# Performance work log

Hardware: AMD Instinct MI355X
Metric: run time of the kernel (lower is better)

## Reference

```python
import jax, jax.numpy as jnp
import numpy as np

N = 50000
E = 800000
D = 64  # d_s


def _mlp2(x, w1, b1, w2, b2):
    # Linear -> SiLU -> Linear
    return jax.nn.silu(x @ w1 + b1) @ w2 + b2


def setup_inputs() -> dict:
    key = jax.random.key(0)
    ks = jax.random.split(key, 20)
    s = jax.random.normal(ks[0], (N, D), jnp.float32)
    v = jax.random.normal(ks[1], (N, 3), jnp.float32)
    edge_index = jax.random.randint(ks[2], (2, E), 0, N, jnp.int32)
    edge_attr = jax.random.normal(ks[3], (E, D), jnp.float32)
    ev = jax.random.normal(ks[4], (E, 3), jnp.float32)
    edge_vec_unit = ev / jnp.linalg.norm(ev, axis=-1, keepdims=True)

    def lin(k, fan_in, fan_out):
        kw, kb = jax.random.split(k)
        lim = 1.0 / np.sqrt(fan_in)
        w = jax.random.uniform(kw, (fan_in, fan_out), jnp.float32, -lim, lim)
        b = jax.random.uniform(kb, (fan_out,), jnp.float32, -lim, lim)
        return w, b

    ng_w1, ng_b1 = lin(ks[5], D + 1, D)
    ng_w2, ng_b2 = lin(ks[6], D, D)
    eg_w1, eg_b1 = lin(ks[7], D + 1, D)
    eg_w2, eg_b2 = lin(ks[8], D, D)
    mg_w1, mg_b1 = lin(ks[9], 3 * D, 2 * D)
    mg_w2, mg_b2 = lin(ks[10], 2 * D, D)
    pe_w, pe_b = lin(ks[11], D, 1)
    up_w, up_b = lin(ks[12], D, D)
    ln_g = jnp.ones((D,), jnp.float32)
    ln_b = jnp.zeros((D,), jnp.float32)
    return dict(s=s, v=v, edge_index=edge_index, edge_attr=edge_attr,
                edge_vec_unit=edge_vec_unit,
                ng_w1=ng_w1, ng_b1=ng_b1, ng_w2=ng_w2, ng_b2=ng_b2,
                eg_w1=eg_w1, eg_b1=eg_b1, eg_w2=eg_w2, eg_b2=eg_b2,
                mg_w1=mg_w1, mg_b1=mg_b1, mg_w2=mg_w2, mg_b2=mg_b2,
                pe_w=pe_w, pe_b=pe_b, up_w=up_w, up_b=up_b,
                ln_g=ln_g, ln_b=ln_b)


def reference(s, v, edge_index, edge_attr, edge_vec_unit,
              ng_w1, ng_b1, ng_w2, ng_b2,
              eg_w1, eg_b1, eg_w2, eg_b2,
              mg_w1, mg_b1, mg_w2, mg_b2,
              pe_w, pe_b, up_w, up_b, ln_g, ln_b):
    row, col = edge_index[0], edge_index[1]
    s_i, s_j = s[row], s[col]            # (E, D)
    v_i, v_j = v[row], v[col]            # (E, 3)

    dot_ij = jnp.sum(v_i * edge_vec_unit, axis=-1, keepdims=True)
    dot_ji = jnp.sum(v_j * -edge_vec_unit, axis=-1, keepdims=True)
    res_ij = 1.0 - dot_ij
    res_ji = 1.0 - dot_ji
    cross_mag = jnp.linalg.norm(jnp.cross(v_i, v_j), axis=-1, keepdims=True)

    node_feat_i = _mlp2(jnp.concatenate([s_i, res_ij], -1), ng_w1, ng_b1, ng_w2, ng_b2)
    node_feat_j = _mlp2(jnp.concatenate([s_j, res_ji], -1), ng_w1, ng_b1, ng_w2, ng_b2)
    edge_feat = _mlp2(jnp.concatenate([edge_attr, cross_mag], -1), eg_w1, eg_b1, eg_w2, eg_b2)

    msg = _mlp2(jnp.concatenate([node_feat_i, node_feat_j, edge_feat], -1),
                mg_w1, mg_b1, mg_w2, mg_b2)   # (E, D)
    coeff = msg @ pe_w + pe_b                 # (E, 1)
    v_msg = edge_vec_unit * coeff             # (E, 3)

    n = s.shape[0]
    s_agg = jax.ops.segment_sum(msg, row, num_segments=n)    # (N, D)
    v_agg = jax.ops.segment_sum(v_msg, row, num_segments=n)  # (N, 3)

    s_new = s + jax.nn.silu(s_agg) @ up_w + up_b
    mu = jnp.mean(s_new, axis=-1, keepdims=True)
    var = jnp.var(s_new, axis=-1, keepdims=True)
    s_out = (s_new - mu) * jax.lax.rsqrt(var + 1e-5) * ln_g + ln_b

    v_new = v + v_agg
    denom = jnp.maximum(jnp.linalg.norm(v_new, axis=-1, keepdims=True), 1e-6)
    v_out = v_new / denom
    return (s_out, v_out)
```

## Files before the change

kernel.cpp:

```cpp
#include <hip/hip_runtime.h>
#include <math.h>

#define NN 50000
#define NE 800000
#define D 64
#define TILE 64

typedef __attribute__((ext_vector_type(8))) short short8;
typedef __attribute__((ext_vector_type(4))) float f32x4;

__device__ __forceinline__ float rdlane(float x, int k) {
  return __uint_as_float(__builtin_amdgcn_readlane(__float_as_uint(x), k));
}
__device__ __forceinline__ float silu_f(float x) { return x / (1.0f + __expf(-x)); }
__device__ __forceinline__ float bfly_sum(float x) {
#pragma unroll
  for (int off = 32; off >= 1; off >>= 1) x += __shfl_xor(x, off, 64);
  return x;
}
__device__ __forceinline__ unsigned short f2bf(float f) {
  unsigned int u = __float_as_uint(f);
  u += 0x7fffu + ((u >> 16) & 1u);
  return (unsigned short)(u >> 16);
}
__device__ __forceinline__ unsigned int pack2(float a, float b) {
  return (unsigned int)f2bf(a) | ((unsigned int)f2bf(b) << 16);
}

__global__ void prep_all(const float* __restrict__ ng_w2,
                         const float* __restrict__ eg_w1,
                         const float* __restrict__ eg_w2,
                         const float* __restrict__ mg_w1,
                         const float* __restrict__ mg_w2,
                         unsigned short* __restrict__ out) {
  int t = blockIdx.x * 256 + threadIdx.x;
  if (t >= 88 * 64) return;
  int frag = t >> 6, L = t & 63;
  const float* W; int K, N, f0;
  if (frag < 8)       { W = ng_w2; K = 64;  N = 64;  f0 = 0; }
  else if (frag < 16) { W = eg_w1; K = 64;  N = 64;  f0 = 8; }
  else if (frag < 24) { W = eg_w2; K = 64;  N = 64;  f0 = 16; }
  else if (frag < 72) { W = mg_w1; K = 192; N = 128; f0 = 24; }
  else                { W = mg_w2; K = 128; N = 64;  f0 = 72; }
  int lf = frag - f0;
  int kd = K >> 5;
  int nt = lf / kd, ks = lf % kd;
  int kb = ks * 32 + (L >> 4) * 8;
  int nc = nt * 16 + (L & 15);
  unsigned int p[4];
#pragma unroll
  for (int jj = 0; jj < 4; ++jj) {
    float a = W[(size_t)(kb + 2 * jj) * N + nc];
    float b = W[(size_t)(kb + 2 * jj + 1) * N + nc];
    p[jj] = pack2(a, b);
  }
  *(uint4*)(out + (size_t)frag * 512 + L * 8) = make_uint4(p[0], p[1], p[2], p[3]);
}

__global__ void node_pre_kernel(const float* __restrict__ s,
                                const float* __restrict__ ng_w1,
                                const float* __restrict__ ng_b1,
                                float* __restrict__ h_ng) {
  int wave = blockIdx.x * (blockDim.x >> 6) + (threadIdx.x >> 6);
  int d = threadIdx.x & 63;
  int n0 = wave * 2;
  if (n0 >= NN) return;
  float x0 = s[(size_t)n0 * D + d];
  float x1 = (n0 + 1 < NN) ? s[(size_t)(n0 + 1) * D + d] : 0.f;
  float b = ng_b1[d];
  float a0 = b, a1 = b;
#pragma unroll 16
  for (int k = 0; k < D; ++k) {
    float w = ng_w1[k * D + d];
    a0 += rdlane(x0, k) * w;
    a1 += rdlane(x1, k) * w;
  }
  h_ng[(size_t)n0 * D + d] = a0;
  if (n0 + 1 < NN) h_ng[(size_t)(n0 + 1) * D + d] = a1;
}

#define OFF_XE 0
#define OFF_AE 9216
#define OFF_A0 0
#define OFF_A1 9216
#define OFF_H  0
#define OFF_C1 18432
#define OFF_ROW 44032
#define OFF_COL 44288
#define OFF_RIJ 44544
#define OFF_RJI 44800
#define OFF_CMG 45056
#define OFF_U   45312
#define OFF_CP  46080
#define SM_SIZE 47104
#define SA 144
#define SC 400
#define SH 272

__global__ __launch_bounds__(256, 3) void edge_mfma(
    const float* __restrict__ v, const int* __restrict__ ei,
    const float* __restrict__ edge_attr, const float* __restrict__ evu,
    const float* __restrict__ ng_w1, const float* __restrict__ ng_b2,
    const float* __restrict__ eg_w1, const float* __restrict__ eg_b1,
    const float* __restrict__ eg_b2,
    const float* __restrict__ mg_b1, const float* __restrict__ mg_b2,
    const float* __restrict__ pe_w, const float* __restrict__ pe_b,
    const float* __restrict__ h_ng,
    const unsigned short* __restrict__ WF,
    float* __restrict__ s_agg, float* __restrict__ v_agg) {
  __shared__ __align__(16) char sm[SM_SIZE];
  int tid = threadIdx.x;
  int w = tid >> 6, lane = tid & 63, l15 = lane & 15, quad = lane >> 4;
  int edge0 = blockIdx.x * TILE;

  short8 F_ng[2], F_e1[2], F_e2[2], F_m1[2][6], F_m2[4];
#pragma unroll
  for (int k = 0; k < 2; ++k) {
    F_ng[k] = *(const short8*)(WF + (size_t)(0 + w * 2 + k) * 512 + lane * 8);
    F_e1[k] = *(const short8*)(WF + (size_t)(8 + w * 2 + k) * 512 + lane * 8);
    F_e2[k] = *(const short8*)(WF + (size_t)(16 + w * 2 + k) * 512 + lane * 8);
  }
#pragma unroll
  for (int n2 = 0; n2 < 2; ++n2)
#pragma unroll
    for (int k = 0; k < 6; ++k)
      F_m1[n2][k] = *(const short8*)(WF + (size_t)(24 + (2 * w + n2) * 6 + k) * 512 + lane * 8);
#pragma unroll
  for (int k = 0; k < 4; ++k)
    F_m2[k] = *(const short8*)(WF + (size_t)(72 + w * 4 + k) * 512 + lane * 8);

  int col = w * 16 + l15;
  float b_ng2 = ng_b2[col];
  float b_e1 = eg_b1[col], b_e2 = eg_b2[col];
  float eglast = eg_w1[64 * 64 + col];
  float b_m1a = mg_b1[w * 32 + l15], b_m1b = mg_b1[w * 32 + 16 + l15];
  float b_m2 = mg_b2[col];
  float pw = pe_w[col];
  float peb = pe_b[0];

  if (tid < 64) {
    int e = tid, ed = edge0 + e;
    int r = ei[ed], c = ei[NE + ed];
    float u0 = evu[ed * 3 + 0], u1 = evu[ed * 3 + 1], u2 = evu[ed * 3 + 2];
    float vi0 = v[r * 3 + 0], vi1 = v[r * 3 + 1], vi2 = v[r * 3 + 2];
    float vj0 = v[c * 3 + 0], vj1 = v[c * 3 + 1], vj2 = v[c * 3 + 2];
    ((int*)(sm + OFF_ROW))[e] = r;
    ((int*)(sm + OFF_COL))[e] = c;
    ((float*)(sm + OFF_RIJ))[e] = 1.0f - (vi0 * u0 + vi1 * u1 + vi2 * u2);
    ((float*)(sm + OFF_RJI))[e] = 1.0f + (vj0 * u0 + vj1 * u1 + vj2 * u2);
    float cx = vi1 * vj2 - vi2 * vj1;
    float cy = vi2 * vj0 - vi0 * vj2;
    float cz = vi0 * vj1 - vi1 * vj0;
    ((float*)(sm + OFF_CMG))[e] = sqrtf(cx * cx + cy * cy + cz * cz);
    ((float*)(sm + OFF_U))[e * 3 + 0] = u0;
    ((float*)(sm + OFF_U))[e * 3 + 1] = u1;
    ((float*)(sm + OFF_U))[e * 3 + 2] = u2;
  }
  {
    int e = tid >> 2, fq = (tid & 3) * 16;
    float va[16];
#pragma unroll
    for (int q = 0; q < 4; ++q) {
      f32x4 x = *(const f32x4*)(edge_attr + (size_t)(edge0 + e) * D + fq + q * 4);
#pragma unroll
      for (int c2 = 0; c2 < 4; ++c2) va[q * 4 + c2] = x[c2];
    }
    *(uint4*)(sm + OFF_XE + e * SA + fq * 2) =
        make_uint4(pack2(va[0], va[1]), pack2(va[2], va[3]), pack2(va[4], va[5]), pack2(va[6], va[7]));
    *(uint4*)(sm + OFF_XE + e * SA + fq * 2 + 16) =
        make_uint4(pack2(va[8], va[9]), pack2(va[10], va[11]), pack2(va[12], va[13]), pack2(va[14], va[15]));
  }
  __syncthreads();

#pragma unroll
  for (int mt = 0; mt < 4; ++mt) {
    f32x4 acc = {0.f, 0.f, 0.f, 0.f};
    short8 a0 = *(const short8*)(sm + OFF_XE + (mt * 16 + l15) * SA + quad * 16);
    short8 a1 = *(const short8*)(sm + OFF_XE + (mt * 16 + l15) * SA + 64 + quad * 16);
    acc = __builtin_amdgcn_mfma_f32_16x16x32_bf16(a0, F_e1[0], acc, 0, 0, 0);
    acc = __builtin_amdgcn_mfma_f32_16x16x32_bf16(a1, F_e1[1], acc, 0, 0, 0);
    int e0 = mt * 16 + quad * 4;
#pragma unroll
    for (int r = 0; r < 4; ++r) {
      float cm = ((const float*)(sm + OFF_CMG))[e0 + r];
      *(unsigned short*)(sm + OFF_AE + (e0 + r) * SA + col * 2) =
          f2bf(silu_f(acc[r] + b_e1 + cm * eglast));
    }
  }
  __syncthreads();

#pragma unroll
  for (int mt = 0; mt < 4; ++mt) {
    f32x4 acc = {0.f, 0.f, 0.f, 0.f};
    short8 a0 = *(const short8*)(sm + OFF_AE + (mt * 16 + l15) * SA + quad * 16);
    short8 a1 = *(const short8*)(sm + OFF_AE + (mt * 16 + l15) * SA + 64 + quad * 16);
    acc = __builtin_amdgcn_mfma_f32_16x16x32_bf16(a0, F_e2[0], acc, 0, 0, 0);
    acc = __builtin_amdgcn_mfma_f32_16x16x32_bf16(a1, F_e2[1], acc, 0, 0, 0);
    int e0 = mt * 16 + quad * 4;
#pragma unroll
    for (int r = 0; r < 4; ++r)
      *(unsigned short*)(sm + OFF_C1 + (e0 + r) * SC + (128 + col) * 2) = f2bf(acc[r] + b_e2);
  }
  __syncthreads();

  {
    int e = tid >> 2, fq = (tid & 3) * 16;
    int rr = ((const int*)(sm + OFF_ROW))[e];
    int cc = ((const int*)(sm + OFF_COL))[e];
    float rij = ((const float*)(sm + OFF_RIJ))[e];
    float rji = ((const float*)(sm + OFF_RJI))[e];
    f32x4 wl[4];
#pragma unroll
    for (int q = 0; q < 4; ++q) wl[q] = *(const f32x4*)(ng_w1 + 64 * 64 + fq + q * 4);

    float va[16];
#pragma unroll
    for (int q = 0; q < 4; ++q) {
      f32x4 h = *(const f32x4*)(h_ng + (size_t)rr * D + fq + q * 4);
#pragma unroll
      for (int c2 = 0; c2 < 4; ++c2) va[q * 4 + c2] = silu_f(h[c2] + rij * wl[q][c2]);
    }
    *(uint4*)(sm + OFF_A0 + e * SA + fq * 2) =
        make_uint4(pack2(va[0], va[1]), pack2(va[2], va[3]), pack2(va[4], va[5]), pack2(va[6], va[7]));
    *(uint4*)(sm + OFF_A0 + e * SA + fq * 2 + 16) =
        make_uint4(pack2(va[8], va[9]), pack2(va[10], va[11]), pack2(va[12], va[13]), pack2(va[14], va[15]));

#pragma unroll
    for (int q = 0; q < 4; ++q) {
      f32x4 h = *(const f32x4*)(h_ng + (size_t)cc * D + fq + q * 4);
#pragma unroll
      for (int c2 = 0; c2 < 4; ++c2) va[q * 4 + c2] = silu_f(h[c2] + rji * wl[q][c2]);
    }
    *(uint4*)(sm + OFF_A1 + e * SA + fq * 2) =
        make_uint4(pack2(va[0], va[1]), pack2(va[2], va[3]), pack2(va[4], va[5]), pack2(va[6], va[7]));
    *(uint4*)(sm + OFF_A1 + e * SA + fq * 2 + 16) =
        make_uint4(pack2(va[8], va[9]), pack2(va[10], va[11]), pack2(va[12], va[13]), pack2(va[14], va[15]));
  }
  __syncthreads();

#pragma unroll
  for (int mt = 0; mt < 4; ++mt) {
    f32x4 acc = {0.f, 0.f, 0.f, 0.f};
    short8 a0 = *(const short8*)(sm + OFF_A0 + (mt * 16 + l15) * SA + quad * 16);
    short8 a1 = *(const short8*)(sm + OFF_A0 + (mt * 16 + l15) * SA + 64 + quad * 16);
    acc = __builtin_amdgcn_mfma_f32_16x16x32_bf16(a0, F_ng[0], acc, 0, 0, 0);
    acc = __builtin_amdgcn_mfma_f32_16x16x32_bf16(a1, F_ng[1], acc, 0, 0, 0);
    int e0 = mt * 16 + quad * 4;
#pragma unroll
    for (int r = 0; r < 4; ++r)
      *(unsigned short*)(sm + OFF_C1 + (e0 + r) * SC + col * 2) = f2bf(acc[r] + b_ng2);
  }
#pragma unroll
  for (int mt = 0; mt < 4; ++mt) {
    f32x4 acc = {0.f, 0.f, 0.f, 0.f};
    short8 a0 = *(const short8*)(sm + OFF_A1 + (mt * 16 + l15) * SA + quad * 16);
    short8 a1 = *(const short8*)(sm + OFF_A1 + (mt * 16 + l15) * SA + 64 + quad * 16);
    acc = __builtin_amdgcn_mfma_f32_16x16x32_bf16(a0, F_ng[0], acc, 0, 0, 0);
    acc = __builtin_amdgcn_mfma_f32_16x16x32_bf16(a1, F_ng[1], acc, 0, 0, 0);
    int e0 = mt * 16 + quad * 4;
#pragma unroll
    for (int r = 0; r < 4; ++r)
      *(unsigned short*)(sm + OFF_C1 + (e0 + r) * SC + (64 + col) * 2) = f2bf(acc[r] + b_ng2);
  }
  __syncthreads();

#pragma unroll
  for (int mt = 0; mt < 4; ++mt) {
    f32x4 acc0 = {0.f, 0.f, 0.f, 0.f};
    f32x4 acc1 = {0.f, 0.f, 0.f, 0.f};
#pragma unroll
    for (int ks = 0; ks < 6; ++ks) {
      short8 a = *(const short8*)(sm + OFF_C1 + (mt * 16 + l15) * SC + ks * 64 + quad * 16);
      acc0 = __builtin_amdgcn_mfma_f32_16x16x32_bf16(a, F_m1[0][ks], acc0, 0, 0, 0);
      acc1 = __builtin_amdgcn_mfma_f32_16x16x32_bf16(a, F_m1[1][ks], acc1, 0, 0, 0);
    }
    int e0 = mt * 16 + quad * 4;
    int ca = w * 32 + l15, cb = w * 32 + 16 + l15;
#pragma unroll
    for (int r = 0; r < 4; ++r) {
      *(unsigned short*)(sm + OFF_H + (e0 + r) * SH + ca * 2) = f2bf(silu_f(acc0[r] + b_m1a));
      *(unsigned short*)(sm + OFF_H + (e0 + r) * SH + cb * 2) = f2bf(silu_f(acc1[r] + b_m1b));
    }
  }
  __syncthreads();

#pragma unroll
  for (int mt = 0; mt < 4; ++mt) {
    f32x4 acc = {0.f, 0.f, 0.f, 0.f};
#pragma unroll
    for (int ks = 0; ks < 4; ++ks) {
      short8 a = *(const short8*)(sm + OFF_H + (mt * 16 + l15) * SH + ks * 64 + quad * 16);
      acc = __builtin_amdgcn_mfma_f32_16x16x32_bf16(a, F_m2[ks], acc, 0, 0, 0);
    }
    int e0 = mt * 16 + quad * 4;
#pragma unroll
    for (int r = 0; r < 4; ++r) {
      float m = acc[r] + b_m2;
      float p = m * pw;
      p += __shfl_xor(p, 1, 64);
      p += __shfl_xor(p, 2, 64);
      p += __shfl_xor(p, 4, 64);
      p += __shfl_xor(p, 8, 64);
      if (l15 == 0) ((float*)(sm + OFF_CP))[(e0 + r) * 4 + w] = p;
      int rn = ((const int*)(sm + OFF_ROW))[e0 + r];
      atomicAdd(&s_agg[(size_t)rn * D + col], m);
    }
  }
  __syncthreads();

  if (tid < 64) {
    const float* cp = (const float*)(sm + OFF_CP);
    float c = cp[tid * 4] + cp[tid * 4 + 1] + cp[tid * 4 + 2] + cp[tid * 4 + 3] + peb;
    int rn = ((const int*)(sm + OFF_ROW))[tid];
    const float* uu = (const float*)(sm + OFF_U);
    atomicAdd(&v_agg[rn * 3 + 0], uu[tid * 3 + 0] * c);
    atomicAdd(&v_agg[rn * 3 + 1], uu[tid * 3 + 1] * c);
    atomicAdd(&v_agg[rn * 3 + 2], uu[tid * 3 + 2] * c);
  }
}

__global__ void node_out_kernel(
    const float* __restrict__ s, const float* __restrict__ v,
    const float* __restrict__ up_w, const float* __restrict__ up_b,
    const float* __restrict__ ln_g, const float* __restrict__ ln_b,
    const float* __restrict__ s_agg, const float* __restrict__ v_agg,
    float* __restrict__ out) {
  int wave = blockIdx.x * (blockDim.x >> 6) + (threadIdx.x >> 6);
  int d = threadIdx.x & 63;
  int n0 = wave * 2;
  if (n0 >= NN) return;
  bool two = (n0 + 1 < NN);

  float g0 = silu_f(s_agg[(size_t)n0 * D + d]);
  float g1 = two ? silu_f(s_agg[(size_t)(n0 + 1) * D + d]) : 0.f;
  float ub = up_b[d];
  float a0 = ub, a1 = ub;
#pragma unroll 16
  for (int k = 0; k < D; ++k) {
    float wv = up_w[k * D + d];
    a0 += rdlane(g0, k) * wv;
    a1 += rdlane(g1, k) * wv;
  }
  float lg = ln_g[d], lb = ln_b[d];
#pragma unroll
  for (int jj = 0; jj < 2; ++jj) {
    int n = n0 + jj;
    if (jj && !two) break;
    float s_new = s[(size_t)n * D + d] + (jj ? a1 : a0);
    float mu = bfly_sum(s_new) * (1.0f / 64.0f);
    float diff = s_new - mu;
    float var = bfly_sum(diff * diff) * (1.0f / 64.0f);
    float inv = 1.0f / sqrtf(var + 1e-5f);
    out[(size_t)n * D + d] = diff * inv * lg + lb;
    if (d < 3) {
      float v0 = v[n * 3 + 0] + v_agg[(size_t)n * 3 + 0];
      float v1 = v[n * 3 + 1] + v_agg[(size_t)n * 3 + 1];
      float v2 = v[n * 3 + 2] + v_agg[(size_t)n * 3 + 2];
      float nrm = sqrtf(v0 * v0 + v1 * v1 + v2 * v2);
      float denom = fmaxf(nrm, 1e-6f);
      float val = (d == 0) ? v0 : ((d == 1) ? v1 : v2);
      out[(size_t)NN * D + (size_t)n * 3 + d] = val / denom;
    }
  }
}

extern "C" void kernel_launch(void* const* d_in, const int* in_sizes, int n_in,
                              void* d_out, int out_size, void* d_ws, size_t ws_size,
                              hipStream_t stream) {
  const float* s         = (const float*)d_in[0];
  const float* v         = (const float*)d_in[1];
  const int*   ei        = (const int*)d_in[2];
  const float* edge_attr = (const float*)d_in[3];
  const float* evu       = (const float*)d_in[4];
  const float* ng_w1     = (const float*)d_in[5];
  const float* ng_b1     = (const float*)d_in[6];
  const float* ng_w2     = (const float*)d_in[7];
  const float* ng_b2     = (const float*)d_in[8];
  const float* eg_w1     = (const float*)d_in[9];
  const float* eg_b1     = (const float*)d_in[10];
  const float* eg_w2     = (const float*)d_in[11];
  const float* eg_b2     = (const float*)d_in[12];
  const float* mg_w1     = (const float*)d_in[13];
  const float* mg_b1     = (const float*)d_in[14];
  const float* mg_w2     = (const float*)d_in[15];
  const float* mg_b2     = (const float*)d_in[16];
  const float* pe_w      = (const float*)d_in[17];
  const float* pe_b      = (const float*)d_in[18];
  const float* up_w      = (const float*)d_in[19];
  const float* up_b      = (const float*)d_in[20];
  const float* ln_g      = (const float*)d_in[21];
  const float* ln_b      = (const float*)d_in[22];
  (void)in_sizes; (void)n_in; (void)out_size; (void)ws_size;

  float* out   = (float*)d_out;
  float* s_agg = (float*)d_ws;
  float* v_agg = s_agg + (size_t)NN * D;
  unsigned short* WF = (unsigned short*)(v_agg + (size_t)NN * 3);
  float* h_ng  = out;

  hipMemsetAsync(d_ws, 0, (size_t)(NN * D + NN * 3) * sizeof(float), stream);

  prep_all<<<22, 256, 0, stream>>>(ng_w2, eg_w1, eg_w2, mg_w1, mg_w2, WF);

  node_pre_kernel<<<(25000 + 3) / 4, 256, 0, stream>>>(s, ng_w1, ng_b1, h_ng);

  edge_mfma<<<NE / TILE, 256, 0, stream>>>(
      v, ei, edge_attr, evu,
      ng_w1, ng_b2, eg_w1, eg_b1, eg_b2,
      mg_b1, mg_b2, pe_w, pe_b, h_ng, WF, s_agg, v_agg);

  node_out_kernel<<<(25000 + 3) / 4, 256, 0, stream>>>(
      s, v, up_w, up_b, ln_g, ln_b, s_agg, v_agg, out);
}
```

Before: 694.5 us.

## Rewrite edge and node kernels as per-wave MFMA pipelines without block syncs

Every kernel is rebuilt. The edge kernel now has each wave own 32 edges end to end. Per-edge features are kept in registers, and the gathered h_ng rows plus edge_attr are loaded straight into MFMA B-fragments, with weights as the A operand. Only wave-private LDS is used, so all __syncthreads go away. The scatter to s_agg is coalesced per row via LDS and readlane. The node pre and post kernels switch from scalar readlane dot products to bf16 MFMA using prepacked ng_w1 and up_w fragments. This aims to cut block-level synchronisation and scalar FMA cost, at the price of more register pressure and bf16 rounding in the node GEMMs.

New measurement: 587.3 us. -15.4%, faster.

```diff
diff --git a/kernel.cpp b/kernel.cpp
--- a/kernel.cpp
+++ b/kernel.cpp
@@ -4,20 +4,11 @@
 #define NN 50000
 #define NE 800000
 #define D 64
-#define TILE 64
 
 typedef __attribute__((ext_vector_type(8))) short short8;
 typedef __attribute__((ext_vector_type(4))) float f32x4;
 
-__device__ __forceinline__ float rdlane(float x, int k) {
-  return __uint_as_float(__builtin_amdgcn_readlane(__float_as_uint(x), k));
-}
 __device__ __forceinline__ float silu_f(float x) { return x / (1.0f + __expf(-x)); }
-__device__ __forceinline__ float bfly_sum(float x) {
-#pragma unroll
-  for (int off = 32; off >= 1; off >>= 1) x += __shfl_xor(x, off, 64);
-  return x;
-}
 __device__ __forceinline__ unsigned short f2bf(float f) {
   unsigned int u = __float_as_uint(f);
   u += 0x7fffu + ((u >> 16) & 1u);
@@ -25,6 +16,14 @@
 }
 __device__ __forceinline__ unsigned int pack2(float a, float b) {
   return (unsigned int)f2bf(a) | ((unsigned int)f2bf(b) << 16);
+}
+__device__ __forceinline__ short8 pack_frag(f32x4 a, f32x4 b) {
+  union { unsigned int u[4]; short8 s; } r;
+  r.u[0] = pack2(a[0], a[1]);
+  r.u[1] = pack2(a[2], a[3]);
+  r.u[2] = pack2(b[0], b[1]);
+  r.u[3] = pack2(b[2], b[3]);
+  return r.s;
 }
 
 __global__ void prep_all(const float* __restrict__ ng_w2,
@@ -32,16 +31,20 @@
                          const float* __restrict__ eg_w2,
                          const float* __restrict__ mg_w1,
                          const float* __restrict__ mg_w2,
+                         const float* __restrict__ ng_w1,
+                         const float* __restrict__ up_w,
                          unsigned short* __restrict__ out) {
   int t = blockIdx.x * 256 + threadIdx.x;
-  if (t >= 88 * 64) return;
+  if (t >= 104 * 64) return;
   int frag = t >> 6, L = t & 63;
   const float* W; int K, N, f0;
   if (frag < 8)       { W = ng_w2; K = 64;  N = 64;  f0 = 0; }
   else if (frag < 16) { W = eg_w1; K = 64;  N = 64;  f0 = 8; }
   else if (frag < 24) { W = eg_w2; K = 64;  N = 64;  f0 = 16; }
   else if (frag < 72) { W = mg_w1; K = 192; N = 128; f0 = 24; }
-  else                { W = mg_w2; K = 128; N = 64;  f0 = 72; }
+  else if (frag < 88) { W = mg_w2; K = 128; N = 64;  f0 = 72; }
+  else if (frag < 96) { W = ng_w1; K = 64;  N = 64;  f0 = 88; }
+  else                { W = up_w;  K = 64;  N = 64;  f0 = 96; }
   int lf = frag - f0;
   int kd = K >> 5;
   int nt = lf / kd, ks = lf % kd;
@@ -57,45 +60,57 @@
   *(uint4*)(out + (size_t)frag * 512 + L * 8) = make_uint4(p[0], p[1], p[2], p[3]);
 }
 
-__global__ void node_pre_kernel(const float* __restrict__ s,
-                                const float* __restrict__ ng_w1,
-                                const float* __restrict__ ng_b1,
-                                float* __restrict__ h_ng) {
-  int wave = blockIdx.x * (blockDim.x >> 6) + (threadIdx.x >> 6);
-  int d = threadIdx.x & 63;
-  int n0 = wave * 2;
-  if (n0 >= NN) return;
-  float x0 = s[(size_t)n0 * D + d];
-  float x1 = (n0 + 1 < NN) ? s[(size_t)(n0 + 1) * D + d] : 0.f;
-  float b = ng_b1[d];
-  float a0 = b, a1 = b;
-#pragma unroll 16
-  for (int k = 0; k < D; ++k) {
-    float w = ng_w1[k * D + d];
-    a0 += rdlane(x0, k) * w;
-    a1 += rdlane(x1, k) * w;
-  }
-  h_ng[(size_t)n0 * D + d] = a0;
-  if (n0 + 1 < NN) h_ng[(size_t)(n0 + 1) * D + d] = a1;
-}
-
-#define OFF_XE 0
-#define OFF_AE 9216
-#define OFF_A0 0
-#define OFF_A1 9216
-#define OFF_H  0
-#define OFF_C1 18432
-#define OFF_ROW 44032
-#define OFF_COL 44288
-#define OFF_RIJ 44544
-#define OFF_RJI 44800
-#define OFF_CMG 45056
-#define OFF_U   45312
-#define OFF_CP  46080
-#define SM_SIZE 47104
-#define SA 144
-#define SC 400
-#define SH 272
+__global__ __launch_bounds__(256, 4) void node_pre(
+    const float* __restrict__ s, const float* __restrict__ ng_b1,
+    const unsigned short* __restrict__ WF, float* __restrict__ h_ng) {
+  __shared__ __align__(16) char sm[4 * 8704];
+  int tid = threadIdx.x, w = tid >> 6, lane = tid & 63;
+  int l15 = lane & 15, q = lane >> 4, fb = q * 8;
+  char* my = sm + w * 8704;
+  int nb = (blockIdx.x * 4 + w) * 32;
+  if (nb >= NN) return;
+
+  short8 Bs[2][2];
+#pragma unroll
+  for (int h = 0; h < 2; ++h)
+#pragma unroll
+    for (int kt = 0; kt < 2; ++kt) {
+      int n = nb + h * 16 + l15; if (n >= NN) n = NN - 1;
+      f32x4 x0 = *(const f32x4*)(s + (size_t)n * D + kt * 32 + fb);
+      f32x4 x1 = *(const f32x4*)(s + (size_t)n * D + kt * 32 + fb + 4);
+      Bs[h][kt] = pack_frag(x0, x1);
+    }
+  short8 F[4][2]; f32x4 bb[4];
+#pragma unroll
+  for (int mt = 0; mt < 4; ++mt) {
+    F[mt][0] = *(const short8*)(WF + (size_t)(88 + mt * 2 + 0) * 512 + lane * 8);
+    F[mt][1] = *(const short8*)(WF + (size_t)(88 + mt * 2 + 1) * 512 + lane * 8);
+    bb[mt] = *(const f32x4*)(ng_b1 + mt * 16 + 4 * q);
+  }
+#pragma unroll
+  for (int h = 0; h < 2; ++h)
+#pragma unroll
+    for (int mt = 0; mt < 4; ++mt) {
+      f32x4 acc = {0.f, 0.f, 0.f, 0.f};
+      acc = __builtin_amdgcn_mfma_f32_16x16x32_bf16(F[mt][0], Bs[h][0], acc, 0, 0, 0);
+      acc = __builtin_amdgcn_mfma_f32_16x16x32_bf16(F[mt][1], Bs[h][1], acc, 0, 0, 0);
+      acc[0] += bb[mt][0]; acc[1] += bb[mt][1]; acc[2] += bb[mt][2]; acc[3] += bb[mt][3];
+      *(f32x4*)(my + (((h * 16 + l15) * 68 + mt * 16 + 4 * q) << 2)) = acc;
+    }
+#pragma unroll
+  for (int h = 0; h < 2; ++h)
+#pragma unroll
+    for (int e = 0; e < 16; ++e) {
+      int n = nb + h * 16 + e;
+      if (n < NN) {
+        float val = *(const float*)(my + (((h * 16 + e) * 68 + lane) << 2));
+        h_ng[(size_t)n * D + lane] = val;
+      }
+    }
+}
+
+#define LSTR 104
+#define LDSW (32 * LSTR * 4)
 
 __global__ __launch_bounds__(256, 3) void edge_mfma(
     const float* __restrict__ v, const int* __restrict__ ei,
@@ -108,258 +123,331 @@
     const float* __restrict__ h_ng,
     const unsigned short* __restrict__ WF,
     float* __restrict__ s_agg, float* __restrict__ v_agg) {
-  __shared__ __align__(16) char sm[SM_SIZE];
-  int tid = threadIdx.x;
-  int w = tid >> 6, lane = tid & 63, l15 = lane & 15, quad = lane >> 4;
-  int edge0 = blockIdx.x * TILE;
-
-  short8 F_ng[2], F_e1[2], F_e2[2], F_m1[2][6], F_m2[4];
-#pragma unroll
-  for (int k = 0; k < 2; ++k) {
-    F_ng[k] = *(const short8*)(WF + (size_t)(0 + w * 2 + k) * 512 + lane * 8);
-    F_e1[k] = *(const short8*)(WF + (size_t)(8 + w * 2 + k) * 512 + lane * 8);
-    F_e2[k] = *(const short8*)(WF + (size_t)(16 + w * 2 + k) * 512 + lane * 8);
-  }
-#pragma unroll
-  for (int n2 = 0; n2 < 2; ++n2)
-#pragma unroll
-    for (int k = 0; k < 6; ++k)
-      F_m1[n2][k] = *(const short8*)(WF + (size_t)(24 + (2 * w + n2) * 6 + k) * 512 + lane * 8);
-#pragma unroll
-  for (int k = 0; k < 4; ++k)
-    F_m2[k] = *(const short8*)(WF + (size_t)(72 + w * 4 + k) * 512 + lane * 8);
-
-  int col = w * 16 + l15;
-  float b_ng2 = ng_b2[col];
-  float b_e1 = eg_b1[col], b_e2 = eg_b2[col];
-  float eglast = eg_w1[64 * 64 + col];
-  float b_m1a = mg_b1[w * 32 + l15], b_m1b = mg_b1[w * 32 + 16 + l15];
-  float b_m2 = mg_b2[col];
-  float pw = pe_w[col];
-  float peb = pe_b[0];
-
-  if (tid < 64) {
-    int e = tid, ed = edge0 + e;
-    int r = ei[ed], c = ei[NE + ed];
-    float u0 = evu[ed * 3 + 0], u1 = evu[ed * 3 + 1], u2 = evu[ed * 3 + 2];
+  __shared__ __align__(16) char sm[4 * LDSW];
+  int tid = threadIdx.x, w = tid >> 6, lane = tid & 63;
+  int l15 = lane & 15, q = lane >> 4, fb = q * 8;
+  char* my = sm + w * LDSW;
+  int eb = (blockIdx.x * 4 + w) * 32;
+
+  int rown[2], coln[2];
+  float rij[2], rji[2], uu0[2], uu1[2], uu2[2], cmag[2];
+#pragma unroll
+  for (int h = 0; h < 2; ++h) {
+    int e = eb + h * 16 + l15;
+    int r = ei[e], c = ei[NE + e];
+    rown[h] = r; coln[h] = c;
+    float u0 = evu[e * 3 + 0], u1 = evu[e * 3 + 1], u2 = evu[e * 3 + 2];
+    uu0[h] = u0; uu1[h] = u1; uu2[h] = u2;
     float vi0 = v[r * 3 + 0], vi1 = v[r * 3 + 1], vi2 = v[r * 3 + 2];
     float vj0 = v[c * 3 + 0], vj1 = v[c * 3 + 1], vj2 = v[c * 3 + 2];
-    ((int*)(sm + OFF_ROW))[e] = r;
-    ((int*)(sm + OFF_COL))[e] = c;
-    ((float*)(sm + OFF_RIJ))[e] = 1.0f - (vi0 * u0 + vi1 * u1 + vi2 * u2);
-    ((float*)(sm + OFF_RJI))[e] = 1.0f + (vj0 * u0 + vj1 * u1 + vj2 * u2);
+    rij[h] = 1.f - (vi0 * u0 + vi1 * u1 + vi2 * u2);
+    rji[h] = 1.f + (vj0 * u0 + vj1 * u1 + vj2 * u2);
     float cx = vi1 * vj2 - vi2 * vj1;
     float cy = vi2 * vj0 - vi0 * vj2;
     float cz = vi0 * vj1 - vi1 * vj0;
-    ((float*)(sm + OFF_CMG))[e] = sqrtf(cx * cx + cy * cy + cz * cz);
-    ((float*)(sm + OFF_U))[e * 3 + 0] = u0;
-    ((float*)(sm + OFF_U))[e * 3 + 1] = u1;
-    ((float*)(sm + OFF_U))[e * 3 + 2] = u2;
-  }
+    cmag[h] = sqrtf(cx * cx + cy * cy + cz * cz);
+  }
+
+  short8 Bai[2][2], Baj[2][2], Bxe[2][2];
+  f32x4 w1l[2][2];
+#pragma unroll
+  for (int kt = 0; kt < 2; ++kt) {
+    w1l[kt][0] = *(const f32x4*)(ng_w1 + 64 * 64 + kt * 32 + fb);
+    w1l[kt][1] = *(const f32x4*)(ng_w1 + 64 * 64 + kt * 32 + fb + 4);
+  }
+#pragma unroll
+  for (int h = 0; h < 2; ++h)
+#pragma unroll
+    for (int kt = 0; kt < 2; ++kt) {
+      const float* pr = h_ng + (size_t)rown[h] * D + kt * 32 + fb;
+      const float* pc = h_ng + (size_t)coln[h] * D + kt * 32 + fb;
+      const float* px = edge_attr + (size_t)(eb + h * 16 + l15) * D + kt * 32 + fb;
+      f32x4 a0 = *(const f32x4*)pr, a1 = *(const f32x4*)(pr + 4);
+      f32x4 b0 = *(const f32x4*)pc, b1 = *(const f32x4*)(pc + 4);
+      f32x4 x0 = *(const f32x4*)px, x1 = *(const f32x4*)(px + 4);
+      f32x4 si0, si1, sj0, sj1;
+#pragma unroll
+      for (int c2 = 0; c2 < 4; ++c2) {
+        si0[c2] = silu_f(a0[c2] + rij[h] * w1l[kt][0][c2]);
+        si1[c2] = silu_f(a1[c2] + rij[h] * w1l[kt][1][c2]);
+        sj0[c2] = silu_f(b0[c2] + rji[h] * w1l[kt][0][c2]);
+        sj1[c2] = silu_f(b1[c2] + rji[h] * w1l[kt][1][c2]);
+      }
+      Bai[h][kt] = pack_frag(si0, si1);
+      Baj[h][kt] = pack_frag(sj0, sj1);
+      Bxe[h][kt] = pack_frag(x0, x1);
+    }
+
   {
-    int e = tid >> 2, fq = (tid & 3) * 16;
-    float va[16];
-#pragma unroll
-    for (int q = 0; q < 4; ++q) {
-      f32x4 x = *(const f32x4*)(edge_attr + (size_t)(edge0 + e) * D + fq + q * 4);
-#pragma unroll
-      for (int c2 = 0; c2 < 4; ++c2) va[q * 4 + c2] = x[c2];
-    }
-    *(uint4*)(sm + OFF_XE + e * SA + fq * 2) =
-        make_uint4(pack2(va[0], va[1]), pack2(va[2], va[3]), pack2(va[4], va[5]), pack2(va[6], va[7]));
-    *(uint4*)(sm + OFF_XE + e * SA + fq * 2 + 16) =
-        make_uint4(pack2(va[8], va[9]), pack2(va[10], va[11]), pack2(va[12], va[13]), pack2(va[14], va[15]));
-  }
-  __syncthreads();
-
+    short8 F[4][2]; f32x4 bb[4];
+#pragma unroll
+    for (int mt = 0; mt < 4; ++mt) {
+      F[mt][0] = *(const short8*)(WF + (size_t)(0 + mt * 2 + 0) * 512 + lane * 8);
+      F[mt][1] = *(const short8*)(WF + (size_t)(0 + mt * 2 + 1) * 512 + lane * 8);
+      bb[mt] = *(const f32x4*)(ng_b2 + mt * 16 + 4 * q);
+    }
+#pragma unroll
+    for (int h = 0; h < 2; ++h)
+#pragma unroll
+      for (int mt = 0; mt < 4; ++mt) {
+        f32x4 ai = {0.f, 0.f, 0.f, 0.f}, aj = {0.f, 0.f, 0.f, 0.f};
+        ai = __builtin_amdgcn_mfma_f32_16x16x32_bf16(F[mt][0], Bai[h][0], ai, 0, 0, 0);
+        ai = __builtin_amdgcn_mfma_f32_16x16x32_bf16(F[mt][1], Bai[h][1], ai, 0, 0, 0);
+        aj = __builtin_amdgcn_mfma_f32_16x16x32_bf16(F[mt][0], Baj[h][0], aj, 0, 0, 0);
+        aj = __builtin_amdgcn_mfma_f32_16x16x32_bf16(F[mt][1], Baj[h][1], aj, 0, 0, 0);
+        uint2 pi, pj;
+        pi.x = pack2(ai[0] + bb[mt][0], ai[1] + bb[mt][1]);
+        pi.y = pack2(ai[2] + bb[mt][2], ai[3] + bb[mt][3]);
+        pj.x = pack2(aj[0] + bb[mt][0], aj[1] + bb[mt][1]);
+        pj.y = pack2(aj[2] + bb[mt][2], aj[3] + bb[mt][3]);
+        int row = h * 16 + l15;
+        *(uint2*)(my + ((row * LSTR + mt * 8 + 2 * q) << 2)) = pi;
+        *(uint2*)(my + ((row * LSTR + 32 + mt * 8 + 2 * q) << 2)) = pj;
+      }
+  }
+
+  {
+    short8 F[4][2]; f32x4 bb[4], el[4];
+#pragma unroll
+    for (int mt = 0; mt < 4; ++mt) {
+      F[mt][0] = *(const short8*)(WF + (size_t)(8 + mt * 2 + 0) * 512 + lane * 8);
+      F[mt][1] = *(const short8*)(WF + (size_t)(8 + mt * 2 + 1) * 512 + lane * 8);
+      bb[mt] = *(const f32x4*)(eg_b1 + mt * 16 + 4 * q);
+      el[mt] = *(const f32x4*)(eg_w1 + 64 * 64 + mt * 16 + 4 * q);
+    }
+#pragma unroll
+    for (int h = 0; h < 2; ++h)
+#pragma unroll
+      for (int mt = 0; mt < 4; ++mt) {
+        f32x4 acc = {0.f, 0.f, 0.f, 0.f};
+        acc = __builtin_amdgcn_mfma_f32_16x16x32_bf16(F[mt][0], Bxe[h][0], acc, 0, 0, 0);
+        acc = __builtin_amdgcn_mfma_f32_16x16x32_bf16(F[mt][1], Bxe[h][1], acc, 0, 0, 0);
+        float t0 = silu_f(acc[0] + bb[mt][0] + cmag[h] * el[mt][0]);
+        float t1 = silu_f(acc[1] + bb[mt][1] + cmag[h] * el[mt][1]);
+        float t2 = silu_f(acc[2] + bb[mt][2] + cmag[h] * el[mt][2]);
+        float t3 = silu_f(acc[3] + bb[mt][3] + cmag[h] * el[mt][3]);
+        uint2 p; p.x = pack2(t0, t1); p.y = pack2(t2, t3);
+        *(uint2*)(my + (((h * 16 + l15) * LSTR + 64 + mt * 8 + 2 * q) << 2)) = p;
+      }
+  }
+
+  {
+    short8 Bae[2][2];
+#pragma unroll
+    for (int h = 0; h < 2; ++h)
+#pragma unroll
+      for (int kt = 0; kt < 2; ++kt)
+        Bae[h][kt] = *(const short8*)(my + (((h * 16 + l15) * LSTR + 64 + 16 * kt + 4 * q) << 2));
+    short8 F[4][2]; f32x4 bb[4];
+#pragma unroll
+    for (int mt = 0; mt < 4; ++mt) {
+      F[mt][0] = *(const short8*)(WF + (size_t)(16 + mt * 2 + 0) * 512 + lane * 8);
+      F[mt][1] = *(const short8*)(WF + (size_t)(16 + mt * 2 + 1) * 512 + lane * 8);
+      bb[mt] = *(const f32x4*)(eg_b2 + mt * 16 + 4 * q);
+    }
+#pragma unroll
+    for (int h = 0; h < 2; ++h)
+#pragma unroll
+      for (int mt = 0; mt < 4; ++mt) {
+        f32x4 acc = {0.f, 0.f, 0.f, 0.f};
+        acc = __builtin_amdgcn_mfma_f32_16x16x32_bf16(F[mt][0], Bae[h][0], acc, 0, 0, 0);
+        acc = __builtin_amdgcn_mfma_f32_16x16x32_bf16(F[mt][1], Bae[h][1], acc, 0, 0, 0);
+        uint2 p;
+        p.x = pack2(acc[0] + bb[mt][0], acc[1] + bb[mt][1]);
+        p.y = pack2(acc[2] + bb[mt][2], acc[3] + bb[mt][3]);
+        *(uint2*)(my + (((h * 16 + l15) * LSTR + 64 + mt * 8 + 2 * q) << 2)) = p;
+      }
+  }
+
+  {
+    short8 Bin[2][6];
+#pragma unroll
+    for (int h = 0; h < 2; ++h)
+#pragma unroll
+      for (int kt = 0; kt < 6; ++kt)
+        Bin[h][kt] = *(const short8*)(my + (((h * 16 + l15) * LSTR + 16 * kt + 4 * q) << 2));
+#pragma unroll
+    for (int mt = 0; mt < 8; ++mt) {
+      short8 F[6];
+#pragma unroll
+      for (int ks = 0; ks < 6; ++ks)
+        F[ks] = *(const short8*)(WF + (size_t)(24 + mt * 6 + ks) * 512 + lane * 8);
+      f32x4 bb = *(const f32x4*)(mg_b1 + mt * 16 + 4 * q);
+#pragma unroll
+      for (int h = 0; h < 2; ++h) {
+        f32x4 acc = {0.f, 0.f, 0.f, 0.f};
+#pragma unroll
+        for (int ks = 0; ks < 6; ++ks)
+          acc = __builtin_amdgcn_mfma_f32_16x16x32_bf16(F[ks], Bin[h][ks], acc, 0, 0, 0);
+        uint2 p;
+        p.x = pack2(silu_f(acc[0] + bb[0]), silu_f(acc[1] + bb[1]));
+        p.y = pack2(silu_f(acc[2] + bb[2]), silu_f(acc[3] + bb[3]));
+        *(uint2*)(my + (((h * 16 + l15) * LSTR + mt * 8 + 2 * q) << 2)) = p;
+      }
+    }
+  }
+
+  f32x4 msg[2][4];
+  {
+    short8 Bh[2][4];
+#pragma unroll
+    for (int h = 0; h < 2; ++h)
+#pragma unroll
+      for (int kt = 0; kt < 4; ++kt)
+        Bh[h][kt] = *(const short8*)(my + (((h * 16 + l15) * LSTR + 16 * kt + 4 * q) << 2));
+#pragma unroll
+    for (int mt = 0; mt < 4; ++mt) {
+      short8 F[4];
+#pragma unroll
+      for (int ks = 0; ks < 4; ++ks)
+        F[ks] = *(const short8*)(WF + (size_t)(72 + mt * 4 + ks) * 512 + lane * 8);
+      f32x4 bb = *(const f32x4*)(mg_b2 + mt * 16 + 4 * q);
+#pragma unroll
+      for (int h = 0; h < 2; ++h) {
+        f32x4 acc = {0.f, 0.f, 0.f, 0.f};
+#pragma unroll
+        for (int ks = 0; ks < 4; ++ks)
+          acc = __builtin_amdgcn_mfma_f32_16x16x32_bf16(F[ks], Bh[h][ks], acc, 0, 0, 0);
+        acc[0] += bb[0]; acc[1] += bb[1]; acc[2] += bb[2]; acc[3] += bb[3];
+        msg[h][mt] = acc;
+      }
+    }
+  }
+
+  float part[2] = {0.f, 0.f};
 #pragma unroll
   for (int mt = 0; mt < 4; ++mt) {
-    f32x4 acc = {0.f, 0.f, 0.f, 0.f};
-    short8 a0 = *(const short8*)(sm + OFF_XE + (mt * 16 + l15) * SA + quad * 16);
-    short8 a1 = *(const short8*)(sm + OFF_XE + (mt * 16 + l15) * SA + 64 + quad * 16);
-    acc = __builtin_amdgcn_mfma_f32_16x16x32_bf16(a0, F_e1[0], acc, 0, 0, 0);
-    acc = __builtin_amdgcn_mfma_f32_16x16x32_bf16(a1, F_e1[1], acc, 0, 0, 0);
-    int e0 = mt * 16 + quad * 4;
-#pragma unroll
-    for (int r = 0; r < 4; ++r) {
-      float cm = ((const float*)(sm + OFF_CMG))[e0 + r];
-      *(unsigned short*)(sm + OFF_AE + (e0 + r) * SA + col * 2) =
-          f2bf(silu_f(acc[r] + b_e1 + cm * eglast));
-    }
-  }
-  __syncthreads();
-
-#pragma unroll
-  for (int mt = 0; mt < 4; ++mt) {
-    f32x4 acc = {0.f, 0.f, 0.f, 0.f};
-    short8 a0 = *(const short8*)(sm + OFF_AE + (mt * 16 + l15) * SA + quad * 16);
-    short8 a1 = *(const short8*)(sm + OFF_AE + (mt * 16 + l15) * SA + 64 + quad * 16);
-    acc = __builtin_amdgcn_mfma_f32_16x16x32_bf16(a0, F_e2[0], acc, 0, 0, 0);
-    acc = __builtin_amdgcn_mfma_f32_16x16x32_bf16(a1, F_e2[1], acc, 0, 0, 0);
-    int e0 = mt * 16 + quad * 4;
-#pragma unroll
-    for (int r = 0; r < 4; ++r)
-      *(unsigned short*)(sm + OFF_C1 + (e0 + r) * SC + (128 + col) * 2) = f2bf(acc[r] + b_e2);
-  }
-  __syncthreads();
-
-  {
-    int e = tid >> 2, fq = (tid & 3) * 16;
-    int rr = ((const int*)(sm + OFF_ROW))[e];
-    int cc = ((const int*)(sm + OFF_COL))[e];
-    float rij = ((const float*)(sm + OFF_RIJ))[e];
-    float rji = ((const float*)(sm + OFF_RJI))[e];
-    f32x4 wl[4];
-#pragma unroll
-    for (int q = 0; q < 4; ++q) wl[q] = *(const f32x4*)(ng_w1 + 64 * 64 + fq + q * 4);
-
-    float va[16];
-#pragma unroll
-    for (int q = 0; q < 4; ++q) {
-      f32x4 h = *(const f32x4*)(h_ng + (size_t)rr * D + fq + q * 4);
-#pragma unroll
-      for (int c2 = 0; c2 < 4; ++c2) va[q * 4 + c2] = silu_f(h[c2] + rij * wl[q][c2]);
-    }
-    *(uint4*)(sm + OFF_A0 + e * SA + fq * 2) =
-        make_uint4(pack2(va[0], va[1]), pack2(va[2], va[3]), pack2(va[4], va[5]), pack2(va[6], va[7]));
-    *(uint4*)(sm + OFF_A0 + e * SA + fq * 2 + 16) =
-        make_uint4(pack2(va[8], va[9]), pack2(va[10], va[11]), pack2(va[12], va[13]), pack2(va[14], va[15]));
-
-#pragma unroll
-    for (int q = 0; q < 4; ++q) {
-      f32x4 h = *(const f32x4*)(h_ng + (size_t)cc * D + fq + q * 4);
-#pragma unroll
-      for (int c2 = 0; c2 < 4; ++c2) va[q * 4 + c2] = silu_f(h[c2] + rji * wl[q][c2]);
-    }
-    *(uint4*)(sm + OFF_A1 + e * SA + fq * 2) =
-        make_uint4(pack2(va[0], va[1]), pack2(va[2], va[3]), pack2(va[4], va[5]), pack2(va[6], va[7]));
-    *(uint4*)(sm + OFF_A1 + e * SA + fq * 2 + 16) =
-        make_uint4(pack2(va[8], va[9]), pack2(va[10], va[11]), pack2(va[12], va[13]), pack2(va[14], va[15]));
-  }
-  __syncthreads();
-
-#pragma unroll
-  for (int mt = 0; mt < 4; ++mt) {
-    f32x4 acc = {0.f, 0.f, 0.f, 0.f};
-    short8 a0 = *(const short8*)(sm + OFF_A0 + (mt * 16 + l15) * SA + quad * 16);
-    short8 a1 = *(const short8*)(sm + OFF_A0 + (mt * 16 + l15) * SA + 64 + quad * 16);
-    acc = __builtin_amdgcn_mfma_f32_16x16x32_bf16(a0, F_ng[0], acc, 0, 0, 0);
-    acc = __builtin_amdgcn_mfma_f32_16x16x32_bf16(a1, F_ng[1], acc, 0, 0, 0);
-    int e0 = mt * 16 + quad * 4;
-#pragma unroll
-    for (int r = 0; r < 4; ++r)
-      *(unsigned short*)(sm + OFF_C1 + (e0 + r) * SC + col * 2) = f2bf(acc[r] + b_ng2);
-  }
-#pragma unroll
-  for (int mt = 0; mt < 4; ++mt) {
-    f32x4 acc = {0.f, 0.f, 0.f, 0.f};
-    short8 a0 = *(const short8*)(sm + OFF_A1 + (mt * 16 + l15) * SA + quad * 16);
-    short8 a1 = *(const short8*)(sm + OFF_A1 + (mt * 16 + l15) * SA + 64 + quad * 16);
-    acc = __builtin_amdgcn_mfma_f32_16x16x32_bf16(a0, F_ng[0], acc, 0, 0, 0);
-    acc = __builtin_amdgcn_mfma_f32_16x16x32_bf16(a1, F_ng[1], acc, 0, 0, 0);
-    int e0 = mt * 16 + quad * 4;
-#pragma unroll
-    for (int r = 0; r < 4; ++r)
-      *(unsigned short*)(sm + OFF_C1 + (e0 + r) * SC + (64 + col) * 2) = f2bf(acc[r] + b_ng2);
-  }
-  __syncthreads();
-
-#pragma unroll
-  for (int mt = 0; mt < 4; ++mt) {
-    f32x4 acc0 = {0.f, 0.f, 0.f, 0.f};
-    f32x4 acc1 = {0.f, 0.f, 0.f, 0.f};
-#pragma unroll
-    for (int ks = 0; ks < 6; ++ks) {
-      short8 a = *(const short8*)(sm + OFF_C1 + (mt * 16 + l15) * SC + ks * 64 + quad * 16);
-      acc0 = __builtin_amdgcn_mfma_f32_16x16x32_bf16(a, F_m1[0][ks], acc0, 0, 0, 0);
-      acc1 = __builtin_amdgcn_mfma_f32_16x16x32_bf16(a, F_m1[1][ks], acc1, 0, 0, 0);
-    }
-    int e0 = mt * 16 + quad * 4;
-    int ca = w * 32 + l15, cb = w * 32 + 16 + l15;
-#pragma unroll
-    for (int r = 0; r < 4; ++r) {
-      *(unsigned short*)(sm + OFF_H + (e0 + r) * SH + ca * 2) = f2bf(silu_f(acc0[r] + b_m1a));
-      *(unsigned short*)(sm + OFF_H + (e0 + r) * SH + cb * 2) = f2bf(silu_f(acc1[r] + b_m1b));
-    }
-  }
-  __syncthreads();
-
-#pragma unroll
-  for (int mt = 0; mt < 4; ++mt) {
-    f32x4 acc = {0.f, 0.f, 0.f, 0.f};
-#pragma unroll
-    for (int ks = 0; ks < 4; ++ks) {
-      short8 a = *(const short8*)(sm + OFF_H + (mt * 16 + l15) * SH + ks * 64 + quad * 16);
-      acc = __builtin_amdgcn_mfma_f32_16x16x32_bf16(a, F_m2[ks], acc, 0, 0, 0);
-    }
-    int e0 = mt * 16 + quad * 4;
-#pragma unroll
-    for (int r = 0; r < 4; ++r) {
-      float m = acc[r] + b_m2;
-      float p = m * pw;
-      p += __shfl_xor(p, 1, 64);
-      p += __shfl_xor(p, 2, 64);
-      p += __shfl_xor(p, 4, 64);
-      p += __shfl_xor(p, 8, 64);
-      if (l15 == 0) ((float*)(sm + OFF_CP))[(e0 + r) * 4 + w] = p;
-      int rn = ((const int*)(sm + OFF_ROW))[e0 + r];
-      atomicAdd(&s_agg[(size_t)rn * D + col], m);
-    }
-  }
-  __syncthreads();
-
-  if (tid < 64) {
-    const float* cp = (const float*)(sm + OFF_CP);
-    float c = cp[tid * 4] + cp[tid * 4 + 1] + cp[tid * 4 + 2] + cp[tid * 4 + 3] + peb;
-    int rn = ((const int*)(sm + OFF_ROW))[tid];
-    const float* uu = (const float*)(sm + OFF_U);
-    atomicAdd(&v_agg[rn * 3 + 0], uu[tid * 3 + 0] * c);
-    atomicAdd(&v_agg[rn * 3 + 1], uu[tid * 3 + 1] * c);
-    atomicAdd(&v_agg[rn * 3 + 2], uu[tid * 3 + 2] * c);
-  }
-}
-
-__global__ void node_out_kernel(
+    f32x4 pw4 = *(const f32x4*)(pe_w + mt * 16 + 4 * q);
+#pragma unroll
+    for (int h = 0; h < 2; ++h)
+      part[h] += msg[h][mt][0] * pw4[0] + msg[h][mt][1] * pw4[1] +
+                 msg[h][mt][2] * pw4[2] + msg[h][mt][3] * pw4[3];
+  }
+  float peb = pe_b[0];
+#pragma unroll
+  for (int h = 0; h < 2; ++h) {
+    part[h] += __shfl_xor(part[h], 16, 64);
+    part[h] += __shfl_xor(part[h], 32, 64);
+    if (q < 3) {
+      float uc = (q == 0) ? uu0[h] : ((q == 1) ? uu1[h] : uu2[h]);
+      atomicAdd(&v_agg[(size_t)rown[h] * 3 + q], uc * (part[h] + peb));
+    }
+  }
+
+#pragma unroll
+  for (int h = 0; h < 2; ++h)
+#pragma unroll
+    for (int mt = 0; mt < 4; ++mt)
+      *(f32x4*)(my + (((h * 16 + l15) * LSTR + mt * 16 + 4 * q) << 2)) = msg[h][mt];
+#pragma unroll
+  for (int h = 0; h < 2; ++h)
+#pragma unroll
+    for (int e = 0; e < 16; ++e) {
+      int sr = __builtin_amdgcn_readlane(rown[h], e);
+      float val = *(const float*)(my + (((h * 16 + e) * LSTR + lane) << 2));
+      atomicAdd(&s_agg[(size_t)sr * D + lane], val);
+    }
+}
+
+__global__ __launch_bounds__(256, 4) void node_out(
     const float* __restrict__ s, const float* __restrict__ v,
-    const float* __restrict__ up_w, const float* __restrict__ up_b,
+    const float* __restrict__ up_b,
     const float* __restrict__ ln_g, const float* __restrict__ ln_b,
     const float* __restrict__ s_agg, const float* __restrict__ v_agg,
-    float* __restrict__ out) {
-  int wave = blockIdx.x * (blockDim.x >> 6) + (threadIdx.x >> 6);
-  int d = threadIdx.x & 63;
-  int n0 = wave * 2;
-  if (n0 >= NN) return;
-  bool two = (n0 + 1 < NN);
-
-  float g0 = silu_f(s_agg[(size_t)n0 * D + d]);
-  float g1 = two ? silu_f(s_agg[(size_t)(n0 + 1) * D + d]) : 0.f;
-  float ub = up_b[d];
-  float a0 = ub, a1 = ub;
-#pragma unroll 16
-  for (int k = 0; k < D; ++k) {
-    float wv = up_w[k * D + d];
-    a0 += rdlane(g0, k) * wv;
-    a1 += rdlane(g1, k) * wv;
-  }
-  float lg = ln_g[d], lb = ln_b[d];
-#pragma unroll
-  for (int jj = 0; jj < 2; ++jj) {
-    int n = n0 + jj;
-    if (jj && !two) break;
-    float s_new = s[(size_t)n * D + d] + (jj ? a1 : a0);
-    float mu = bfly_sum(s_new) * (1.0f / 64.0f);
-    float diff = s_new - mu;
-    float var = bfly_sum(diff * diff) * (1.0f / 64.0f);
-    float inv = 1.0f / sqrtf(var + 1e-5f);
-    out[(size_t)n * D + d] = diff * inv * lg + lb;
-    if (d < 3) {
+    const unsigned short* __restrict__ WF, float* __restrict__ out) {
+  __shared__ __align__(16) char sm[4 * 8704];
+  int tid = threadIdx.x, w = tid >> 6, lane = tid & 63;
+  int l15 = lane & 15, q = lane >> 4, fb = q * 8;
+  char* my = sm + w * 8704;
+  int nb = (blockIdx.x * 4 + w) * 32;
+  if (nb >= NN) return;
+
+  short8 Bg[2][2];
+#pragma unroll
+  for (int h = 0; h < 2; ++h)
+#pragma unroll
+    for (int kt = 0; kt < 2; ++kt) {
+      int n = nb + h * 16 + l15; if (n >= NN) n = NN - 1;
+      f32x4 g0 = *(const f32x4*)(s_agg + (size_t)n * D + kt * 32 + fb);
+      f32x4 g1 = *(const f32x4*)(s_agg + (size_t)n * D + kt * 32 + fb + 4);
+#pragma unroll
+      for (int c2 = 0; c2 < 4; ++c2) { g0[c2] = silu_f(g0[c2]); g1[c2] = silu_f(g1[c2]); }
+      Bg[h][kt] = pack_frag(g0, g1);
+    }
+  short8 F[4][2]; f32x4 bb[4];
+#pragma unroll
+  for (int mt = 0; mt < 4; ++mt) {
+    F[mt][0] = *(const short8*)(WF + (size_t)(96 + mt * 2 + 0) * 512 + lane * 8);
+    F[mt][1] = *(const short8*)(WF + (size_t)(96 + mt * 2 + 1) * 512 + lane * 8);
+    bb[mt] = *(const f32x4*)(up_b + mt * 16 + 4 * q);
+  }
+  f32x4 sn[2][4];
+#pragma unroll
+  for (int h = 0; h < 2; ++h) {
+    int n = nb + h * 16 + l15; if (n >= NN) n = NN - 1;
+#pragma unroll
+    for (int mt = 0; mt < 4; ++mt) {
+      f32x4 acc = {0.f, 0.f, 0.f, 0.f};
+      acc = __builtin_amdgcn_mfma_f32_16x16x32_bf16(F[mt][0], Bg[h][0], acc, 0, 0, 0);
+      acc = __builtin_amdgcn_mfma_f32_16x16x32_bf16(F[mt][1], Bg[h][1], acc, 0, 0, 0);
+      f32x4 sv = *(const f32x4*)(s + (size_t)n * D + mt * 16 + 4 * q);
+      sn[h][mt][0] = acc[0] + bb[mt][0] + sv[0];
+      sn[h][mt][1] = acc[1] + bb[mt][1] + sv[1];
+      sn[h][mt][2] = acc[2] + bb[mt][2] + sv[2];
+      sn[h][mt][3] = acc[3] + bb[mt][3] + sv[3];
+    }
+  }
+#pragma unroll
+  for (int h = 0; h < 2; ++h) {
+    float m = 0.f;
+#pragma unroll
+    for (int mt = 0; mt < 4; ++mt)
+      m += sn[h][mt][0] + sn[h][mt][1] + sn[h][mt][2] + sn[h][mt][3];
+    m += __shfl_xor(m, 16, 64);
+    m += __shfl_xor(m, 32, 64);
+    float mu = m * (1.f / 64.f);
+    float vv = 0.f;
+#pragma unroll
+    for (int mt = 0; mt < 4; ++mt)
+#pragma unroll
+      for (int r = 0; r < 4; ++r) {
+        float d = sn[h][mt][r] - mu;
+        vv += d * d;
+      }
+    vv += __shfl_xor(vv, 16, 64);
+    vv += __shfl_xor(vv, 32, 64);
+    float inv = 1.f / sqrtf(vv * (1.f / 64.f) + 1e-5f);
+#pragma unroll
+    for (int mt = 0; mt < 4; ++mt) {
+      f32x4 lg = *(const f32x4*)(ln_g + mt * 16 + 4 * q);
+      f32x4 lb = *(const f32x4*)(ln_b + mt * 16 + 4 * q);
+      f32x4 ov;
+#pragma unroll
+      for (int r = 0; r < 4; ++r) ov[r] = (sn[h][mt][r] - mu) * inv * lg[r] + lb[r];
+      *(f32x4*)(my + (((h * 16 + l15) * 68 + mt * 16 + 4 * q) << 2)) = ov;
+    }
+  }
+#pragma unroll
+  for (int h = 0; h < 2; ++h)
+#pragma unroll
+    for (int e = 0; e < 16; ++e) {
+      int n = nb + h * 16 + e;
+      if (n < NN) {
+        float val = *(const float*)(my + (((h * 16 + e) * 68 + lane) << 2));
+        out[(size_t)n * D + lane] = val;
+      }
+    }
+#pragma unroll
+  for (int h = 0; h < 2; ++h) {
+    int n = nb + h * 16 + l15;
+    if (q < 3 && n < NN) {
       float v0 = v[n * 3 + 0] + v_agg[(size_t)n * 3 + 0];
       float v1 = v[n * 3 + 1] + v_agg[(size_t)n * 3 + 1];
       float v2 = v[n * 3 + 2] + v_agg[(size_t)n * 3 + 2];
       float nrm = sqrtf(v0 * v0 + v1 * v1 + v2 * v2);
       float denom = fmaxf(nrm, 1e-6f);
-      float val = (d == 0) ? v0 : ((d == 1) ? v1 : v2);
-      out[(size_t)NN * D + (size_t)n * 3 + d] = val / denom;
+      float val = (q == 0) ? v0 : ((q == 1) ? v1 : v2);
+      out[(size_t)NN * D + (size_t)n * 3 + q] = val / denom;
     }
   }
 }
@@ -400,15 +488,16 @@
 
   hipMemsetAsync(d_ws, 0, (size_t)(NN * D + NN * 3) * sizeof(float), stream);
 
-  prep_all<<<22, 256, 0, stream>>>(ng_w2, eg_w1, eg_w2, mg_w1, mg_w2, WF);
-
-  node_pre_kernel<<<(25000 + 3) / 4, 256, 0, stream>>>(s, ng_w1, ng_b1, h_ng);
-
-  edge_mfma<<<NE / TILE, 256, 0, stream>>>(
+  prep_all<<<26, 256, 0, stream>>>(ng_w2, eg_w1, eg_w2, mg_w1, mg_w2, ng_w1, up_w, WF);
+
+  int node_blocks = (NN + 127) / 128;
+  node_pre<<<node_blocks, 256, 0, stream>>>(s, ng_b1, WF, h_ng);
+
+  edge_mfma<<<NE / 128, 256, 0, stream>>>(
       v, ei, edge_attr, evu,
       ng_w1, ng_b2, eg_w1, eg_b1, eg_b2,
       mg_b1, mg_b2, pe_w, pe_b, h_ng, WF, s_agg, v_agg);
 
-  node_out_kernel<<<(25000 + 3) / 4, 256, 0, stream>>>(
-      s, v, up_w, up_b, ln_g, ln_b, s_agg, v_agg, out);
-}
+  node_out<<<node_blocks, 256, 0, stream>>>(
+      s, v, up_b, ln_g, ln_b, s_agg, v_agg, WF, out);
+}
```
